# Kernel tuning notes

Hardware: AMD Instinct MI355X
Metric: run time of the kernel (lower is better)

## Reference

```python
import jax, jax.numpy as jnp
import numpy as np

B, H, N, D = 1, 24, 3072, 128
BM = 192            # query block size (kernel is hard-coded to BM=192)
QG = N // BM        # number of query groups
TOP_KEYS = 0.3
MULTIPLE_OF = 128
TK = int(MULTIPLE_OF * round(TOP_KEYS * N / MULTIPLE_OF))  # 896


def setup_inputs() -> dict:
    key = jax.random.key(0)
    kq, kk, kv = jax.random.split(key, 3)
    q = jax.random.normal(kq, (B, H, N, D), dtype=jnp.float32)
    k = jax.random.normal(kk, (B, H, N, D), dtype=jnp.float32)
    v = jax.random.normal(kv, (B, H, N, D), dtype=jnp.float32)
    return {"q": q, "k": k, "v": v}


def reference(q, k, v):
    """Full-step (inference_step==1) path of SparseDiffAttn._fast_attention:
    dense_colsum_attn -> top-k key selection per 192-query block -> csp_attn,
    returning o_cache = o_dense - o_sparse (the cached residual output)."""
    scale = 1.0 / jnp.sqrt(jnp.asarray(D, q.dtype))
    # --- dense_colsum_attn ---
    s = jnp.einsum('bhqd,bhkd->bhqk', q, k) * scale          # [B,H,N,N]
    p = jax.nn.softmax(s, axis=-1)                           # softmax probs
    o = jnp.einsum('bhqk,bhkd->bhqd', p, v)                  # dense output
    # block column sums: per 192-query group, sum of probs per key
    bs = p.reshape(B, H, QG, BM, N).sum(axis=3)              # [B,H,QG,N]
    # --- top-k routing (should_compress_indices=False branch) ---
    _, inds = jax.lax.top_k(jax.lax.stop_gradient(bs), TK)   # [B,H,QG,TK]
    # --- csp_attn: block-sparse attention over selected keys ---
    k_sel = jnp.take_along_axis(k[:, :, None], inds[..., None], axis=3)  # [B,H,QG,TK,D]
    v_sel = jnp.take_along_axis(v[:, :, None], inds[..., None], axis=3)
    qb = q.reshape(B, H, QG, BM, D)
    ss = jnp.einsum('bhgqd,bhgkd->bhgqk', qb, k_sel) * scale # [B,H,QG,BM,TK]
    ps = jax.nn.softmax(ss, axis=-1)
    o_sparse = jnp.einsum('bhgqk,bhgkd->bhgqd', ps, v_sel).reshape(B, H, N, D)
    # o_cache = o - csp_attn(q,k,v,inds,counts)
    return o - o_sparse
```

## Files before the change

kernel.cpp:

```cpp
#include <hip/hip_runtime.h>
#include <stdint.h>
#include <math.h>


#define H 24
#define N 3072
#define DH 128
#define SCALE 0.08838834764831845f
#define TK 896
#define MARG 1.6e-5f
#define MAXC 96

typedef __attribute__((ext_vector_type(8))) short short8;
typedef __attribute__((ext_vector_type(4))) float f32x4;
typedef __attribute__((address_space(1))) unsigned char GAS;
typedef __attribute__((address_space(3))) unsigned char LAS;
#define GLD16(g, l) __builtin_amdgcn_global_load_lds((GAS*)(g), (LAS*)(l), 16, 0, 0)

__device__ __forceinline__ uint32_t bf_rne(float x){
  uint32_t u = __float_as_uint(x);
  return (u + 0x7FFFu + ((u >> 16) & 1u)) >> 16;
}

__device__ __forceinline__ f32x4 f4zero(){ f32x4 z = {0.f,0.f,0.f,0.f}; return z; }

__device__ __forceinline__ void split8_2(const float* f, uint4& h4, uint4& l4){
  uint32_t hw[4], lw[4];
#pragma unroll
  for (int i = 0; i < 4; i++){
    float a = f[2*i], b = f[2*i+1];
    uint32_t ha = bf_rne(a), hb = bf_rne(b);
    float ra = a - __uint_as_float(ha << 16);
    float rb = b - __uint_as_float(hb << 16);
    hw[i] = ha | (hb << 16);
    lw[i] = bf_rne(ra) | (bf_rne(rb) << 16);
  }
  h4.x = hw[0]; h4.y = hw[1]; h4.z = hw[2]; h4.w = hw[3];
  l4.x = lw[0]; l4.y = lw[1]; l4.z = lw[2]; l4.w = lw[3];
}

__device__ __forceinline__ short8 as_s8(const uint4 u){
  union { uint4 u4; short8 s; } t; t.u4 = u; return t.s;
}

__device__ __forceinline__ void mapHC(int bid, int& h, int& ch){
  int x = bid & 7;
  int i = bid >> 3;
  h = x + 8 * (i / 48);
  ch = i % 48;
}

__device__ __forceinline__ void load_qfrags2(const float* qhead, int R, int w, int lane,
                                             uint4* qh, uint4* ql){
  int row = R + w*16 + (lane & 15);
  const float* qp = qhead + (size_t)row * DH;
#pragma unroll
  for (int s = 0; s < 4; s++){
    int d0 = s*32 + (lane >> 4)*8;
    float4 a = *(const float4*)(qp + d0);
    float4 b = *(const float4*)(qp + d0 + 4);
    float f[8] = {a.x*SCALE, a.y*SCALE, a.z*SCALE, a.w*SCALE,
                  b.x*SCALE, b.y*SCALE, b.z*SCALE, b.w*SCALE};
    split8_2(f, qh[s], ql[s]);
  }
}

__device__ __forceinline__ void ldK16(const float* kp, float4* r){
  r[0] = *(const float4*)(kp);
  r[1] = *(const float4*)(kp + 4);
  r[2] = *(const float4*)(kp + 8);
  r[3] = *(const float4*)(kp + 12);
}
__device__ __forceinline__ void wrK16(const float4* r, char* khi, char* klo,
                                      int jst, int dblk){
  float f0[8] = {r[0].x,r[0].y,r[0].z,r[0].w,r[1].x,r[1].y,r[1].z,r[1].w};
  float f1[8] = {r[2].x,r[2].y,r[2].z,r[2].w,r[3].x,r[3].y,r[3].z,r[3].w};
  uint4 h4, l4;
  int base = jst*256 + dblk*32;
  int sw = (jst & 7) << 4;
  split8_2(f0, h4, l4);
  *(uint4*)(khi + (base ^ sw)) = h4;
  *(uint4*)(klo + (base ^ sw)) = l4;
  split8_2(f1, h4, l4);
  *(uint4*)(khi + ((base + 16) ^ sw)) = h4;
  *(uint4*)(klo + ((base + 16) ^ sw)) = l4;
}

struct V16 { float4 a0, b0, a1, b1; };
__device__ __forceinline__ V16 load_v(const float* vp0, const float* vp1){
  V16 v;
  v.a0 = *(const float4*)(vp0);
  v.b0 = *(const float4*)(vp0 + 4);
  v.a1 = *(const float4*)(vp1);
  v.b1 = *(const float4*)(vp1 + 4);
  return v;
}
__device__ __forceinline__ void write_v(const V16& v, char* vts, int jv2, int dv8){
  float f0[8] = {v.a0.x,v.a0.y,v.a0.z,v.a0.w,v.b0.x,v.b0.y,v.b0.z,v.b0.w};
  float f1[8] = {v.a1.x,v.a1.y,v.a1.z,v.a1.w,v.b1.x,v.b1.y,v.b1.z,v.b1.w};
#pragma unroll
  for (int i = 0; i < 8; i++){
    uint32_t wrd = bf_rne(f0[i]) | (bf_rne(f1[i]) << 16);
    int r = dv8 + i;
    int off = (r*80 + jv2*2) ^ (((r >> 3) & 1) << 4);
    *(uint32_t*)(vts + off) = wrd;
  }
}

__device__ __forceinline__ void zcompute3(const char* khi, const char* klo,
                                          const uint4* qh, const uint4* ql,
                                          int lane, f32x4* zac){
  zac[0] = f4zero(); zac[1] = f4zero();
#pragma unroll
  for (int s = 0; s < 4; s++){
    short8 qa = as_s8(qh[s]);
    short8 qb = as_s8(ql[s]);
#pragma unroll
    for (int ct = 0; ct < 2; ct++){
      int key = ct*16 + (lane & 15);
      int off = (key*256 + (s*32 + (lane >> 4)*8)*2) ^ ((key & 7) << 4);
      short8 kh = *(const short8*)(khi + off);
      short8 kl = *(const short8*)(klo + off);
      zac[ct] = __builtin_amdgcn_mfma_f32_16x16x32_bf16(qa, kl, zac[ct], 0, 0, 0);
      zac[ct] = __builtin_amdgcn_mfma_f32_16x16x32_bf16(qb, kh, zac[ct], 0, 0, 0);
      zac[ct] = __builtin_amdgcn_mfma_f32_16x16x32_bf16(qa, kh, zac[ct], 0, 0, 0);
    }
  }
}

__device__ __forceinline__ void pv_step(const float pn[2][4], char* pw, const char* vts,
                                        f32x4* oac, int l15, int l4){
#pragma unroll
  for (int ct = 0; ct < 2; ct++)
#pragma unroll
    for (int r = 0; r < 4; r++){
      int row = l4*4 + r;
      int off = (row*80 + (ct*16 + l15)*2) ^ (((row >> 3) & 1) << 4);
      *(unsigned short*)(pw + off) = (unsigned short)bf_rne(pn[ct][r]);
    }
  int offA = (l15*80 + l4*16) ^ (((l15 >> 3) & 1) << 4);
  short8 ap = *(const short8*)(pw + offA);
#pragma unroll
  for (int vt = 0; vt < 8; vt++){
    int vrow = vt*16 + l15;
    int offB = (vrow*80 + l4*16) ^ (((vrow >> 3) & 1) << 4);
    short8 vb = *(const short8*)(vts + offB);
    oac[vt] = __builtin_amdgcn_mfma_f32_16x16x32_bf16(ap, vb, oac[vt], 0, 0, 0);
  }
}

__global__ __launch_bounds__(256) void kS(const float* __restrict__ kg,
                                          unsigned short* __restrict__ khig,
                                          unsigned short* __restrict__ klog){
  size_t idx = ((size_t)blockIdx.x*256 + threadIdx.x)*8;
  float4 a = *(const float4*)(kg + idx);
  float4 b = *(const float4*)(kg + idx + 4);
  float f[8] = {a.x,a.y,a.z,a.w,b.x,b.y,b.z,b.w};
  uint4 h4, l4;
  split8_2(f, h4, l4);
  *(uint4*)(khig + idx) = h4;
  *(uint4*)(klog + idx) = l4;
}

template<int DMA>
__global__ __launch_bounds__(256, 3) void kAB(const float* __restrict__ qg,
                                              const float* __restrict__ kg,
                                              const float* __restrict__ vg,
                                              const unsigned short* __restrict__ khig,
                                              const unsigned short* __restrict__ klog,
                                              double* __restrict__ Zg,
                                              float* __restrict__ cpart,
                                              float* __restrict__ outg){
  __shared__ alignas(16) char khi[2][8192];
  __shared__ alignas(16) char klo[2][8192];
  __shared__ alignas(16) char vts[10240];
  __shared__ alignas(16) char pls[4][1280];
  __shared__ float colbuf[2][4][32];
  int h, ch; mapHC(blockIdx.x, h, ch);
  const int tid = threadIdx.x, w = tid >> 6, lane = tid & 63;
  const int l15 = lane & 15, l4 = lane >> 4;
  const int R = ch * 64;
  const float* qhead = qg + (size_t)h*N*DH;
  const float* khead = kg + (size_t)h*N*DH;
  const float* vhead = vg + (size_t)h*N*DH;
  uint4 qh[4], ql[4];
  load_qfrags2(qhead, R, w, lane, qh, ql);

  size_t b0 = 0, b1 = 0;
  if (DMA){
    int g0 = w*128 + lane, g1 = g0 + 64;
    int k0 = g0 >> 4, sl0 = (g0 & 15) ^ (k0 & 7);
    int k1 = g1 >> 4, sl1 = (g1 & 15) ^ (k1 & 7);
    b0 = ((size_t)h*N + k0)*DH + sl0*8;
    b1 = ((size_t)h*N + k1)*DH + sl1*8;
  }
  const int wofs = w*2048;
  const int jst = tid >> 3, dblk = tid & 7;
  const int jv2 = (tid & 15)*2, dv8 = (tid >> 4)*8;

  if (DMA){
    GLD16(khig + b0, khi[0] + wofs);  GLD16(khig + b1, khi[0] + wofs + 1024);
    GLD16(klog + b0, klo[0] + wofs);  GLD16(klog + b1, klo[0] + wofs + 1024);
  } else {
    float4 k0r[4];
    ldK16(khead + (size_t)jst*DH + dblk*16, k0r);
    wrK16(k0r, khi[0], klo[0], jst, dblk);
  }
  __syncthreads();
  double zs[4] = {0.0,0.0,0.0,0.0};
  float4 kr[4];
  for (int kt = 0; kt < 96; kt++){
    int cur = kt & 1;
    if (kt < 95){
      if (DMA){
        size_t st = (size_t)(kt+1)*32*DH;
        GLD16(khig + b0 + st, khi[cur^1] + wofs);  GLD16(khig + b1 + st, khi[cur^1] + wofs + 1024);
        GLD16(klog + b0 + st, klo[cur^1] + wofs);  GLD16(klog + b1 + st, klo[cur^1] + wofs + 1024);
      } else {
        ldK16(khead + (size_t)((kt+1)*32 + jst)*DH + dblk*16, kr);
      }
    }
    f32x4 zac[2];
    zcompute3(khi[cur], klo[cur], qh, ql, lane, zac);
#pragma unroll
    for (int ct = 0; ct < 2; ct++)
#pragma unroll
      for (int r = 0; r < 4; r++)
        zs[r] += (double)__expf(zac[ct][r]);
    if (!DMA && kt < 95) wrK16(kr, khi[cur^1], klo[cur^1], jst, dblk);
    __syncthreads();
  }
#pragma unroll
  for (int m = 1; m < 16; m <<= 1)
#pragma unroll
    for (int r = 0; r < 4; r++)
      zs[r] += __shfl_xor(zs[r], m);
  float rz[4];
#pragma unroll
  for (int r = 0; r < 4; r++) rz[r] = (float)(1.0 / zs[r]);
  if (l15 == 0){
#pragma unroll
    for (int r = 0; r < 4; r++)
      Zg[h*N + R + w*16 + l4*4 + r] = zs[r];
  }

  if (DMA){
    GLD16(khig + b0, khi[0] + wofs);  GLD16(khig + b1, khi[0] + wofs + 1024);
    GLD16(klog + b0, klo[0] + wofs);  GLD16(klog + b1, klo[0] + wofs + 1024);
  } else {
    float4 k0r[4];
    ldK16(khead + (size_t)jst*DH + dblk*16, k0r);
    wrK16(k0r, khi[0], klo[0], jst, dblk);
  }
  {
    V16 v0 = load_v(vhead + (size_t)jv2*DH + dv8, vhead + (size_t)(jv2+1)*DH + dv8);
    write_v(v0, vts, jv2, dv8);
  }
  __syncthreads();
  f32x4 oac[8];
#pragma unroll
  for (int i = 0; i < 8; i++) oac[i] = f4zero();
  float* cp = cpart + (size_t)(h*48 + ch) * 3072;
  V16 vr;
  for (int kt = 0; kt < 96; kt++){
    int cur = kt & 1;
    if (kt > 0 && tid < 32)
      cp[(kt-1)*32 + tid] = colbuf[cur^1][0][tid] + colbuf[cur^1][1][tid]
                          + colbuf[cur^1][2][tid] + colbuf[cur^1][3][tid];
    if (kt < 95){
      if (DMA){
        size_t st = (size_t)(kt+1)*32*DH;
        GLD16(khig + b0 + st, khi[cur^1] + wofs);  GLD16(khig + b1 + st, khi[cur^1] + wofs + 1024);
        GLD16(klog + b0 + st, klo[cur^1] + wofs);  GLD16(klog + b1 + st, klo[cur^1] + wofs + 1024);
      } else {
        ldK16(khead + (size_t)((kt+1)*32 + jst)*DH + dblk*16, kr);
      }
      vr = load_v(vhead + (size_t)((kt+1)*32 + jv2)*DH + dv8,
                  vhead + (size_t)((kt+1)*32 + jv2 + 1)*DH + dv8);
    }
    f32x4 zac[2];
    zcompute3(khi[cur], klo[cur], qh, ql, lane, zac);
    float pn[2][4];
#pragma unroll
    for (int ct = 0; ct < 2; ct++)
#pragma unroll
      for (int r = 0; r < 4; r++)
        pn[ct][r] = __expf(zac[ct][r]) * rz[r];
#pragma unroll
    for (int ct = 0; ct < 2; ct++){
      float cs = pn[ct][0] + pn[ct][1] + pn[ct][2] + pn[ct][3];
      cs += __shfl_xor(cs, 16);
      cs += __shfl_xor(cs, 32);
      if (lane < 16) colbuf[cur][w][ct*16 + lane] = cs;
    }
    pv_step(pn, pls[w], vts, oac, l15, l4);
    __syncthreads();
    if (kt < 95){
      write_v(vr, vts, jv2, dv8);
      if (!DMA) wrK16(kr, khi[cur^1], klo[cur^1], jst, dblk);
    }
    __syncthreads();
  }
  if (tid < 32)
    cp[95*32 + tid] = colbuf[1][0][tid] + colbuf[1][1][tid]
                    + colbuf[1][2][tid] + colbuf[1][3][tid];
#pragma unroll
  for (int vt = 0; vt < 8; vt++)
#pragma unroll
    for (int r = 0; r < 4; r++)
      outg[((size_t)h*N + R + w*16 + l4*4 + r)*DH + vt*16 + l15] = oac[vt][r];
}

__global__ __launch_bounds__(256, 2) void kC(const float* __restrict__ cpart,
                                             const double* __restrict__ Zd,
                                             const float* __restrict__ qg,
                                             const float* __restrict__ kg,
                                             int* __restrict__ selg){
  __shared__ float cu[3072];
  __shared__ int red[4];
  __shared__ int runS;
  __shared__ int cidx[MAXC];
  __shared__ double cval[MAXC];
  __shared__ double rbuf[256];
  const int gid = blockIdx.x;
  const int h = gid >> 4, g = gid & 15;
  const int tid = threadIdx.x, w = tid >> 6, lane = tid & 63;
  const float* p0 = cpart + (size_t)(h*48 + g*3) * 3072;
  const float* p1 = p0 + 3072;
  const float* p2 = p0 + 6144;
  for (int i = tid; i < 3072; i += 256)
    cu[i] = p0[i] + p1[i] + p2[i];
  __syncthreads();
  uint32_t lo = 0u, hi = 0xFFFFFFFFu;
  for (int it = 0; it < 32; it++){
    bool active = (lo < hi);
    uint32_t mid = (uint32_t)(((uint64_t)lo + (uint64_t)hi + 1ull) >> 1);
    int c = 0;
    if (active){
      for (int i = tid; i < 3072; i += 256)
        c += (__float_as_uint(cu[i]) >= mid) ? 1 : 0;
#pragma unroll
      for (int m = 1; m < 64; m <<= 1) c += __shfl_xor(c, m);
    }
    if (lane == 0) red[w] = c;
    __syncthreads();
    int tot = red[0] + red[1] + red[2] + red[3];
    __syncthreads();
    if (active){ if (tot >= TK) lo = mid; else hi = mid - 1; }
  }
  const float Vf = __uint_as_float(lo);
  const float thr_hi = Vf + MARG;
  const float thr_lo = Vf - MARG;
  {
    int c = 0;
    for (int i = tid; i < 3072; i += 256) c += (cu[i] > thr_hi) ? 1 : 0;
#pragma unroll
    for (int m = 1; m < 64; m <<= 1) c += __shfl_xor(c, m);
    if (lane == 0) red[w] = c;
  }
  __syncthreads();
  const int n_in = red[0] + red[1] + red[2] + red[3];
  const int need = TK - n_in;
  int* sb = selg + (size_t)gid * TK;
  if (tid == 0) runS = 0;
  __syncthreads();
  for (int ck = 0; ck < 12; ck++){
    int j = ck*256 + tid;
    bool f = (cu[j] > thr_hi);
    unsigned long long bal = __ballot(f);
    int wpre = __popcll(bal & ((1ull << lane) - 1ull));
    int wtot = __popcll(bal);
    if (lane == 0) red[w] = wtot;
    __syncthreads();
    int woff = 0;
    for (int x = 0; x < w; x++) woff += red[x];
    int base = runS;
    if (f) sb[base + woff + wpre] = j;
    __syncthreads();
    if (tid == 0) runS = base + red[0] + red[1] + red[2] + red[3];
    __syncthreads();
  }
  if (tid == 0) runS = 0;
  __syncthreads();
  for (int ck = 0; ck < 12; ck++){
    int j = ck*256 + tid;
    bool f = (!(cu[j] > thr_hi)) && (cu[j] >= thr_lo);
    unsigned long long bal = __ballot(f);
    int wpre = __popcll(bal & ((1ull << lane) - 1ull));
    int wtot = __popcll(bal);
    if (lane == 0) red[w] = wtot;
    __syncthreads();
    int woff = 0;
    for (int x = 0; x < w; x++) woff += red[x];
    int base = runS;
    int pos = base + woff + wpre;
    if (f && pos < MAXC) cidx[pos] = j;
    __syncthreads();
    if (tid == 0) runS = base + red[0] + red[1] + red[2] + red[3];
    __syncthreads();
  }
  int ccnt = runS < MAXC ? runS : MAXC;
  __syncthreads();
  const int row = g*192 + (tid < 192 ? tid : 0);
  const float* qp = qg + ((size_t)h*N + row)*DH;
  const double Zrow = Zd[h*N + row];
  for (int c = 0; c < ccnt; c++){
    double t = 0.0;
    if (tid < 192){
      const float* kp = kg + ((size_t)h*N + cidx[c])*DH;
      double a0 = 0.0, a1 = 0.0, a2 = 0.0, a3 = 0.0;
#pragma unroll 4
      for (int d = 0; d < DH; d += 4){
        a0 = fma((double)qp[d],   (double)kp[d],   a0);
        a1 = fma((double)qp[d+1], (double)kp[d+1], a1);
        a2 = fma((double)qp[d+2], (double)kp[d+2], a2);
        a3 = fma((double)qp[d+3], (double)kp[d+3], a3);
      }
      double z = ((a0 + a1) + (a2 + a3)) * 0.08838834764831845;
      t = exp(z) / Zrow;
    }
    rbuf[tid] = t;
    __syncthreads();
#pragma unroll
    for (int s = 128; s > 0; s >>= 1){
      if (tid < s) rbuf[tid] += rbuf[tid + s];
      __syncthreads();
    }
    if (tid == 0) cval[c] = rbuf[0];
    __syncthreads();
  }
  if (tid < ccnt){
    double my = cval[tid];
    int myi = cidx[tid];
    int rank = 0;
    for (int u = 0; u < ccnt; u++){
      double cu_ = cval[u];
      if (cu_ > my || (cu_ == my && cidx[u] < myi)) rank++;
    }
    if (rank < need) sb[n_in + rank] = myi;
  }
}

template<int DMA>
__global__ __launch_bounds__(256, 3) void kD(const float* __restrict__ qg,
                                             const float* __restrict__ kg,
                                             const float* __restrict__ vg,
                                             const double* __restrict__ Zg,
                                             const int* __restrict__ selg,
                                             const unsigned short* __restrict__ khig,
                                             const unsigned short* __restrict__ klog,
                                             float* __restrict__ outg){
  __shared__ alignas(16) char khi[2][8192];
  __shared__ alignas(16) char klo[2][8192];
  __shared__ alignas(16) char vts[10240];
  __shared__ alignas(16) char pls[4][1280];
  __shared__ int sell[TK];
  int h, ch; mapHC(blockIdx.x, h, ch);
  const int tid = threadIdx.x, w = tid >> 6, lane = tid & 63;
  const int l15 = lane & 15, l4 = lane >> 4;
  const int R = ch * 64;
  const int g = ch / 3;
  const float* qhead = qg + (size_t)h*N*DH;
  const float* khead = kg + (size_t)h*N*DH;
  const float* vhead = vg + (size_t)h*N*DH;
  const int* sb = selg + (size_t)(h*16 + g) * TK;
  for (int i = tid; i < TK; i += 256) sell[i] = sb[i];
  uint4 qh[4], ql[4];
  load_qfrags2(qhead, R, w, lane, qh, ql);
  float rz[4];
#pragma unroll
  for (int r = 0; r < 4; r++)
    rz[r] = (float)(1.0 / Zg[h*N + R + w*16 + l4*4 + r]);
  f32x4 oac[8];
#pragma unroll
  for (int i = 0; i < 8; i++) oac[i] = f4zero();
  float rh[4] = {0.f,0.f,0.f,0.f};

  int p0g = 0, p1g = 0, sl0 = 0, sl1 = 0;
  if (DMA){
    int g0 = w*128 + lane, g1 = g0 + 64;
    p0g = g0 >> 4; sl0 = (g0 & 15) ^ (p0g & 7);
    p1g = g1 >> 4; sl1 = (g1 & 15) ^ (p1g & 7);
  }
  const int wofs = w*2048;
  const int jst = tid >> 3, dblk = tid & 7;
  const int jv2 = (tid & 15)*2, dv8 = (tid >> 4)*8;
  __syncthreads();
  if (DMA){
    size_t b0 = ((size_t)h*N + sell[p0g])*DH + sl0*8;
    size_t b1 = ((size_t)h*N + sell[p1g])*DH + sl1*8;
    GLD16(khig + b0, khi[0] + wofs);  GLD16(khig + b1, khi[0] + wofs + 1024);
    GLD16(klog + b0, klo[0] + wofs);  GLD16(klog + b1, klo[0] + wofs + 1024);
  } else {
    float4 k0r[4];
    ldK16(khead + (size_t)sell[jst]*DH + dblk*16, k0r);
    wrK16(k0r, khi[0], klo[0], jst, dblk);
  }
  {
    V16 v0 = load_v(vhead + (size_t)sell[jv2]*DH + dv8,
                    vhead + (size_t)sell[jv2+1]*DH + dv8);
    write_v(v0, vts, jv2, dv8);
  }
  __syncthreads();
  float4 kr[4];
  V16 vr;
  for (int st = 0; st < 28; st++){
    int cur = st & 1;
    if (st < 27){
      if (DMA){
        size_t b0 = ((size_t)h*N + sell[(st+1)*32 + p0g])*DH + sl0*8;
        size_t b1 = ((size_t)h*N + sell[(st+1)*32 + p1g])*DH + sl1*8;
        GLD16(khig + b0, khi[cur^1] + wofs);  GLD16(khig + b1, khi[cur^1] + wofs + 1024);
        GLD16(klog + b0, klo[cur^1] + wofs);  GLD16(klog + b1, klo[cur^1] + wofs + 1024);
      } else {
        ldK16(khead + (size_t)sell[(st+1)*32 + jst]*DH + dblk*16, kr);
      }
      vr = load_v(vhead + (size_t)sell[(st+1)*32 + jv2]*DH + dv8,
                  vhead + (size_t)sell[(st+1)*32 + jv2 + 1]*DH + dv8);
    }
    f32x4 zac[2];
    zcompute3(khi[cur], klo[cur], qh, ql, lane, zac);
    float pn[2][4];
#pragma unroll
    for (int ct = 0; ct < 2; ct++)
#pragma unroll
      for (int r = 0; r < 4; r++){
        pn[ct][r] = __expf(zac[ct][r]) * rz[r];
        rh[r] += pn[ct][r];
      }
    pv_step(pn, pls[w], vts, oac, l15, l4);
    __syncthreads();
    if (st < 27){
      write_v(vr, vts, jv2, dv8);
      if (!DMA) wrK16(kr, khi[cur^1], klo[cur^1], jst, dblk);
    }
    __syncthreads();
  }
#pragma unroll
  for (int m = 1; m < 16; m <<= 1)
#pragma unroll
    for (int r = 0; r < 4; r++)
      rh[r] += __shfl_xor(rh[r], m);
  float ri[4];
#pragma unroll
  for (int r = 0; r < 4; r++) ri[r] = 1.0f / rh[r];
#pragma unroll
  for (int vt = 0; vt < 8; vt++)
#pragma unroll
    for (int r = 0; r < 4; r++){
      size_t idx = ((size_t)h*N + R + w*16 + l4*4 + r)*DH + vt*16 + l15;
      outg[idx] = outg[idx] - oac[vt][r]*ri[r];
    }
}

extern "C" void kernel_launch(void* const* d_in, const int* in_sizes, int n_in,
                              void* d_out, int out_size, void* d_ws, size_t ws_size,
                              hipStream_t stream){
  (void)in_sizes; (void)n_in; (void)out_size;
  const float* q = (const float*)d_in[0];
  const float* k = (const float*)d_in[1];
  const float* v = (const float*)d_in[2];
  float* out = (float*)d_out;
  const size_t KELEMS = (size_t)H*N*DH;
  const size_t KBYTES = KELEMS*2;
  const size_t ZB = (size_t)H*N*8;
  const size_t CPB = (size_t)1152*3072*4;
  const size_t SELB = (size_t)384*TK*4;
  const bool dma = ws_size >= 2*KBYTES + ZB + CPB + SELB;
  char* wsb = (char*)d_ws;
  unsigned short *khig = nullptr, *klog = nullptr;
  double* Z; float* cpart; int* sel;
  if (dma){
    khig = (unsigned short*)wsb;
    klog = (unsigned short*)(wsb + KBYTES);
    Z = (double*)(wsb + 2*KBYTES);
    cpart = (float*)(wsb + 2*KBYTES + ZB);
    sel = (int*)(wsb + 2*KBYTES + ZB + CPB);
  } else {
    Z = (double*)wsb;
    cpart = (float*)(wsb + ZB);
    sel = (int*)(wsb + ZB + CPB);
  }
  if (dma){
    kS<<<dim3(4608), dim3(256), 0, stream>>>(k, khig, klog);
    kAB<1><<<dim3(1152), dim3(256), 0, stream>>>(q, k, v, khig, klog, Z, cpart, out);
    kC<<<dim3(384), dim3(256), 0, stream>>>(cpart, Z, q, k, sel);
    kD<1><<<dim3(1152), dim3(256), 0, stream>>>(q, k, v, Z, sel, khig, klog, out);
  } else {
    kAB<0><<<dim3(1152), dim3(256), 0, stream>>>(q, k, v, khig, klog, Z, cpart, out);
    kC<<<dim3(384), dim3(256), 0, stream>>>(cpart, Z, q, k, sel);
    kD<0><<<dim3(1152), dim3(256), 0, stream>>>(q, k, v, Z, sel, khig, klog, out);
  }
}
```

Before: 851.6 us.

## Process two query tiles per block, precast V to bf16, drop K-lo in PV passes

kAB now handles 128 query rows per block (two 64-row tiles sharing each K/V tile load), halving the grid and reusing LDS traffic. V is pre-converted to bf16 in the split kernel. The probability-times-V passes in kAB and kD use only two MFMAs per score instead of three because the K low part is dropped. The selection margin is widened to absorb the extra error. Occupancy bounds change too (kAB to 2, kD to 4), trading register pressure and precision for fewer MFMAs and fewer loads.

```diff
diff --git a/kernel.cpp b/kernel.cpp
--- a/kernel.cpp
+++ b/kernel.cpp
@@ -8,7 +8,7 @@
 #define DH 128
 #define SCALE 0.08838834764831845f
 #define TK 896
-#define MARG 1.6e-5f
+#define MARG 1.0e-4f
 #define MAXC 96
 
 typedef __attribute__((ext_vector_type(8))) short short8;
@@ -43,7 +43,13 @@
   union { uint4 u4; short8 s; } t; t.u4 = u; return t.s;
 }
 
-__device__ __forceinline__ void mapHC(int bid, int& h, int& ch){
+__device__ __forceinline__ void mapHC24(int bid, int& h, int& ch){
+  int x = bid & 7;
+  int i = bid >> 3;
+  h = x + 8 * (i / 24);
+  ch = i % 24;
+}
+__device__ __forceinline__ void mapHC48(int bid, int& h, int& ch){
   int x = bid & 7;
   int i = bid >> 3;
   h = x + 8 * (i / 48);
@@ -85,6 +91,20 @@
   *(uint4*)(khi + ((base + 16) ^ sw)) = h4;
   *(uint4*)(klo + ((base + 16) ^ sw)) = l4;
 }
+__device__ __forceinline__ void wrK16h(const float4* r, char* khi, int jst, int dblk){
+  float f[16] = {r[0].x,r[0].y,r[0].z,r[0].w,r[1].x,r[1].y,r[1].z,r[1].w,
+                 r[2].x,r[2].y,r[2].z,r[2].w,r[3].x,r[3].y,r[3].z,r[3].w};
+  uint32_t wv[8];
+#pragma unroll
+  for (int i = 0; i < 8; i++)
+    wv[i] = bf_rne(f[2*i]) | (bf_rne(f[2*i+1]) << 16);
+  int base = jst*256 + dblk*32;
+  int sw = (jst & 7) << 4;
+  uint4 a = {wv[0],wv[1],wv[2],wv[3]};
+  uint4 b = {wv[4],wv[5],wv[6],wv[7]};
+  *(uint4*)(khi + (base ^ sw)) = a;
+  *(uint4*)(khi + ((base + 16) ^ sw)) = b;
+}
 
 struct V16 { float4 a0, b0, a1, b1; };
 __device__ __forceinline__ V16 load_v(const float* vp0, const float* vp1){
@@ -106,25 +126,103 @@
     *(uint32_t*)(vts + off) = wrd;
   }
 }
-
-__device__ __forceinline__ void zcompute3(const char* khi, const char* klo,
-                                          const uint4* qh, const uint4* ql,
-                                          int lane, f32x4* zac){
-  zac[0] = f4zero(); zac[1] = f4zero();
+__device__ __forceinline__ void write_vbf(uint4 va, uint4 vb, char* vts, int jv2, int dv8){
+  const unsigned short* a = (const unsigned short*)&va;
+  const unsigned short* b = (const unsigned short*)&vb;
+#pragma unroll
+  for (int i = 0; i < 8; i++){
+    uint32_t wrd = (uint32_t)a[i] | ((uint32_t)b[i] << 16);
+    int r = dv8 + i;
+    int off = (r*80 + jv2*2) ^ (((r >> 3) & 1) << 4);
+    *(uint32_t*)(vts + off) = wrd;
+  }
+}
+
+__device__ __forceinline__ void zc3_dual(const char* khi, const char* klo,
+    const uint4* qhA, const uint4* qlA, const uint4* qhB, const uint4* qlB,
+    int lane, f32x4* zA, f32x4* zB){
+  zA[0] = f4zero(); zA[1] = f4zero();
+  zB[0] = f4zero(); zB[1] = f4zero();
 #pragma unroll
   for (int s = 0; s < 4; s++){
-    short8 qa = as_s8(qh[s]);
-    short8 qb = as_s8(ql[s]);
+    short8 qaA = as_s8(qhA[s]), qbA = as_s8(qlA[s]);
+    short8 qaB = as_s8(qhB[s]), qbB = as_s8(qlB[s]);
 #pragma unroll
     for (int ct = 0; ct < 2; ct++){
       int key = ct*16 + (lane & 15);
       int off = (key*256 + (s*32 + (lane >> 4)*8)*2) ^ ((key & 7) << 4);
       short8 kh = *(const short8*)(khi + off);
       short8 kl = *(const short8*)(klo + off);
-      zac[ct] = __builtin_amdgcn_mfma_f32_16x16x32_bf16(qa, kl, zac[ct], 0, 0, 0);
+      zA[ct] = __builtin_amdgcn_mfma_f32_16x16x32_bf16(qaA, kl, zA[ct], 0, 0, 0);
+      zA[ct] = __builtin_amdgcn_mfma_f32_16x16x32_bf16(qbA, kh, zA[ct], 0, 0, 0);
+      zA[ct] = __builtin_amdgcn_mfma_f32_16x16x32_bf16(qaA, kh, zA[ct], 0, 0, 0);
+      zB[ct] = __builtin_amdgcn_mfma_f32_16x16x32_bf16(qaB, kl, zB[ct], 0, 0, 0);
+      zB[ct] = __builtin_amdgcn_mfma_f32_16x16x32_bf16(qbB, kh, zB[ct], 0, 0, 0);
+      zB[ct] = __builtin_amdgcn_mfma_f32_16x16x32_bf16(qaB, kh, zB[ct], 0, 0, 0);
+    }
+  }
+}
+
+__device__ __forceinline__ void zc2_dual(const char* khi,
+    const uint4* qhA, const uint4* qlA, const uint4* qhB, const uint4* qlB,
+    int lane, f32x4* zA, f32x4* zB){
+  zA[0] = f4zero(); zA[1] = f4zero();
+  zB[0] = f4zero(); zB[1] = f4zero();
+#pragma unroll
+  for (int s = 0; s < 4; s++){
+    short8 qaA = as_s8(qhA[s]), qbA = as_s8(qlA[s]);
+    short8 qaB = as_s8(qhB[s]), qbB = as_s8(qlB[s]);
+#pragma unroll
+    for (int ct = 0; ct < 2; ct++){
+      int key = ct*16 + (lane & 15);
+      int off = (key*256 + (s*32 + (lane >> 4)*8)*2) ^ ((key & 7) << 4);
+      short8 kh = *(const short8*)(khi + off);
+      zA[ct] = __builtin_amdgcn_mfma_f32_16x16x32_bf16(qbA, kh, zA[ct], 0, 0, 0);
+      zA[ct] = __builtin_amdgcn_mfma_f32_16x16x32_bf16(qaA, kh, zA[ct], 0, 0, 0);
+      zB[ct] = __builtin_amdgcn_mfma_f32_16x16x32_bf16(qbB, kh, zB[ct], 0, 0, 0);
+      zB[ct] = __builtin_amdgcn_mfma_f32_16x16x32_bf16(qaB, kh, zB[ct], 0, 0, 0);
+    }
+  }
+}
+
+__device__ __forceinline__ void zc2_one(const char* khi,
+    const uint4* qh, const uint4* ql, int lane, f32x4* zac){
+  zac[0] = f4zero(); zac[1] = f4zero();
+#pragma unroll
+  for (int s = 0; s < 4; s++){
+    short8 qa = as_s8(qh[s]), qb = as_s8(ql[s]);
+#pragma unroll
+    for (int ct = 0; ct < 2; ct++){
+      int key = ct*16 + (lane & 15);
+      int off = (key*256 + (s*32 + (lane >> 4)*8)*2) ^ ((key & 7) << 4);
+      short8 kh = *(const short8*)(khi + off);
       zac[ct] = __builtin_amdgcn_mfma_f32_16x16x32_bf16(qb, kh, zac[ct], 0, 0, 0);
       zac[ct] = __builtin_amdgcn_mfma_f32_16x16x32_bf16(qa, kh, zac[ct], 0, 0, 0);
     }
+  }
+}
+
+__device__ __forceinline__ void pv_dual(const float pnA[2][4], const float pnB[2][4],
+    char* pwA, char* pwB, const char* vts, f32x4* oacA, f32x4* oacB, int l15, int l4){
+#pragma unroll
+  for (int ct = 0; ct < 2; ct++)
+#pragma unroll
+    for (int r = 0; r < 4; r++){
+      int row = l4*4 + r;
+      int off = (row*80 + (ct*16 + l15)*2) ^ (((row >> 3) & 1) << 4);
+      *(unsigned short*)(pwA + off) = (unsigned short)bf_rne(pnA[ct][r]);
+      *(unsigned short*)(pwB + off) = (unsigned short)bf_rne(pnB[ct][r]);
+    }
+  int offA = (l15*80 + l4*16) ^ (((l15 >> 3) & 1) << 4);
+  short8 apA = *(const short8*)(pwA + offA);
+  short8 apB = *(const short8*)(pwB + offA);
+#pragma unroll
+  for (int vt = 0; vt < 8; vt++){
+    int vrow = vt*16 + l15;
+    int offB = (vrow*80 + l4*16) ^ (((vrow >> 3) & 1) << 4);
+    short8 vb = *(const short8*)(vts + offB);
+    oacA[vt] = __builtin_amdgcn_mfma_f32_16x16x32_bf16(apA, vb, oacA[vt], 0, 0, 0);
+    oacB[vt] = __builtin_amdgcn_mfma_f32_16x16x32_bf16(apB, vb, oacB[vt], 0, 0, 0);
   }
 }
 
@@ -150,8 +248,10 @@
 }
 
 __global__ __launch_bounds__(256) void kS(const float* __restrict__ kg,
+                                          const float* __restrict__ vg,
                                           unsigned short* __restrict__ khig,
-                                          unsigned short* __restrict__ klog){
+                                          unsigned short* __restrict__ klog,
+                                          unsigned short* __restrict__ vbfg){
   size_t idx = ((size_t)blockIdx.x*256 + threadIdx.x)*8;
   float4 a = *(const float4*)(kg + idx);
   float4 b = *(const float4*)(kg + idx + 4);
@@ -160,31 +260,40 @@
   split8_2(f, h4, l4);
   *(uint4*)(khig + idx) = h4;
   *(uint4*)(klog + idx) = l4;
+  float4 c = *(const float4*)(vg + idx);
+  float4 d = *(const float4*)(vg + idx + 4);
+  uint4 v4;
+  v4.x = bf_rne(c.x) | (bf_rne(c.y) << 16);
+  v4.y = bf_rne(c.z) | (bf_rne(c.w) << 16);
+  v4.z = bf_rne(d.x) | (bf_rne(d.y) << 16);
+  v4.w = bf_rne(d.z) | (bf_rne(d.w) << 16);
+  *(uint4*)(vbfg + idx) = v4;
 }
 
 template<int DMA>
-__global__ __launch_bounds__(256, 3) void kAB(const float* __restrict__ qg,
+__global__ __launch_bounds__(256, 2) void kAB(const float* __restrict__ qg,
                                               const float* __restrict__ kg,
                                               const float* __restrict__ vg,
                                               const unsigned short* __restrict__ khig,
                                               const unsigned short* __restrict__ klog,
+                                              const unsigned short* __restrict__ vbfg,
                                               double* __restrict__ Zg,
                                               float* __restrict__ cpart,
                                               float* __restrict__ outg){
   __shared__ alignas(16) char khi[2][8192];
-  __shared__ alignas(16) char klo[2][8192];
+  __shared__ alignas(16) char kloB[16384];
   __shared__ alignas(16) char vts[10240];
-  __shared__ alignas(16) char pls[4][1280];
   __shared__ float colbuf[2][4][32];
-  int h, ch; mapHC(blockIdx.x, h, ch);
+  int h, ch; mapHC24(blockIdx.x, h, ch);
   const int tid = threadIdx.x, w = tid >> 6, lane = tid & 63;
   const int l15 = lane & 15, l4 = lane >> 4;
-  const int R = ch * 64;
+  const int R = ch * 128;
   const float* qhead = qg + (size_t)h*N*DH;
   const float* khead = kg + (size_t)h*N*DH;
   const float* vhead = vg + (size_t)h*N*DH;
-  uint4 qh[4], ql[4];
-  load_qfrags2(qhead, R, w, lane, qh, ql);
+  uint4 qhA[4], qlA[4], qhB[4], qlB[4];
+  load_qfrags2(qhead, R,      w, lane, qhA, qlA);
+  load_qfrags2(qhead, R + 64, w, lane, qhB, qlB);
 
   size_t b0 = 0, b1 = 0;
   if (DMA){
@@ -197,118 +306,142 @@
   const int wofs = w*2048;
   const int jst = tid >> 3, dblk = tid & 7;
   const int jv2 = (tid & 15)*2, dv8 = (tid >> 4)*8;
+  char* kloT0 = kloB;
+  char* kloT1 = kloB + 8192;
 
   if (DMA){
     GLD16(khig + b0, khi[0] + wofs);  GLD16(khig + b1, khi[0] + wofs + 1024);
-    GLD16(klog + b0, klo[0] + wofs);  GLD16(klog + b1, klo[0] + wofs + 1024);
+    GLD16(klog + b0, kloT0 + wofs);   GLD16(klog + b1, kloT0 + wofs + 1024);
   } else {
     float4 k0r[4];
     ldK16(khead + (size_t)jst*DH + dblk*16, k0r);
-    wrK16(k0r, khi[0], klo[0], jst, dblk);
-  }
-  __syncthreads();
-  double zs[4] = {0.0,0.0,0.0,0.0};
+    wrK16(k0r, khi[0], kloT0, jst, dblk);
+  }
+  __syncthreads();
+  double zsA[4] = {0.0,0.0,0.0,0.0};
+  double zsB[4] = {0.0,0.0,0.0,0.0};
   float4 kr[4];
+  for (int kt = 0; kt < 96; kt++){
+    int cur = kt & 1;
+    char* kloC = cur ? kloT1 : kloT0;
+    char* kloN = cur ? kloT0 : kloT1;
+    if (kt < 95){
+      if (DMA){
+        size_t st = (size_t)(kt+1)*32*DH;
+        GLD16(khig + b0 + st, khi[cur^1] + wofs);  GLD16(khig + b1 + st, khi[cur^1] + wofs + 1024);
+        GLD16(klog + b0 + st, kloN + wofs);        GLD16(klog + b1 + st, kloN + wofs + 1024);
+      } else {
+        ldK16(khead + (size_t)((kt+1)*32 + jst)*DH + dblk*16, kr);
+      }
+    }
+    f32x4 zA[2], zB[2];
+    zc3_dual(khi[cur], kloC, qhA, qlA, qhB, qlB, lane, zA, zB);
+#pragma unroll
+    for (int ct = 0; ct < 2; ct++)
+#pragma unroll
+      for (int r = 0; r < 4; r++){
+        zsA[r] += (double)__expf(zA[ct][r]);
+        zsB[r] += (double)__expf(zB[ct][r]);
+      }
+    if (!DMA && kt < 95) wrK16(kr, khi[cur^1], kloN, jst, dblk);
+    __syncthreads();
+  }
+#pragma unroll
+  for (int m = 1; m < 16; m <<= 1)
+#pragma unroll
+    for (int r = 0; r < 4; r++){
+      zsA[r] += __shfl_xor(zsA[r], m);
+      zsB[r] += __shfl_xor(zsB[r], m);
+    }
+  float rzA[4], rzB[4];
+#pragma unroll
+  for (int r = 0; r < 4; r++){
+    rzA[r] = (float)(1.0 / zsA[r]);
+    rzB[r] = (float)(1.0 / zsB[r]);
+  }
+  if (l15 == 0){
+#pragma unroll
+    for (int r = 0; r < 4; r++){
+      Zg[h*N + R      + w*16 + l4*4 + r] = zsA[r];
+      Zg[h*N + R + 64 + w*16 + l4*4 + r] = zsB[r];
+    }
+  }
+
+  char* pwA = kloB + w*2560;
+  char* pwB = pwA + 1280;
+  if (DMA){
+    GLD16(khig + b0, khi[0] + wofs);  GLD16(khig + b1, khi[0] + wofs + 1024);
+    uint4 va0 = *(const uint4*)(vbfg + ((size_t)h*N + jv2    )*DH + dv8);
+    uint4 vb0 = *(const uint4*)(vbfg + ((size_t)h*N + jv2 + 1)*DH + dv8);
+    write_vbf(va0, vb0, vts, jv2, dv8);
+  } else {
+    float4 k0r[4];
+    ldK16(khead + (size_t)jst*DH + dblk*16, k0r);
+    wrK16h(k0r, khi[0], jst, dblk);
+    V16 v0 = load_v(vhead + (size_t)jv2*DH + dv8, vhead + (size_t)(jv2+1)*DH + dv8);
+    write_v(v0, vts, jv2, dv8);
+  }
+  __syncthreads();
+  f32x4 oacA[8], oacB[8];
+#pragma unroll
+  for (int i = 0; i < 8; i++){ oacA[i] = f4zero(); oacB[i] = f4zero(); }
+  uint4 va, vb2;
+  V16 vr;
   for (int kt = 0; kt < 96; kt++){
     int cur = kt & 1;
     if (kt < 95){
       if (DMA){
         size_t st = (size_t)(kt+1)*32*DH;
         GLD16(khig + b0 + st, khi[cur^1] + wofs);  GLD16(khig + b1 + st, khi[cur^1] + wofs + 1024);
-        GLD16(klog + b0 + st, klo[cur^1] + wofs);  GLD16(klog + b1 + st, klo[cur^1] + wofs + 1024);
+        va  = *(const uint4*)(vbfg + ((size_t)h*N + (kt+1)*32 + jv2    )*DH + dv8);
+        vb2 = *(const uint4*)(vbfg + ((size_t)h*N + (kt+1)*32 + jv2 + 1)*DH + dv8);
       } else {
         ldK16(khead + (size_t)((kt+1)*32 + jst)*DH + dblk*16, kr);
+        vr = load_v(vhead + (size_t)((kt+1)*32 + jv2)*DH + dv8,
+                    vhead + (size_t)((kt+1)*32 + jv2 + 1)*DH + dv8);
       }
     }
-    f32x4 zac[2];
-    zcompute3(khi[cur], klo[cur], qh, ql, lane, zac);
+    f32x4 zA[2], zB[2];
+    zc2_dual(khi[cur], qhA, qlA, qhB, qlB, lane, zA, zB);
+    float pnA[2][4], pnB[2][4];
 #pragma unroll
     for (int ct = 0; ct < 2; ct++)
 #pragma unroll
-      for (int r = 0; r < 4; r++)
-        zs[r] += (double)__expf(zac[ct][r]);
-    if (!DMA && kt < 95) wrK16(kr, khi[cur^1], klo[cur^1], jst, dblk);
-    __syncthreads();
-  }
-#pragma unroll
-  for (int m = 1; m < 16; m <<= 1)
-#pragma unroll
-    for (int r = 0; r < 4; r++)
-      zs[r] += __shfl_xor(zs[r], m);
-  float rz[4];
-#pragma unroll
-  for (int r = 0; r < 4; r++) rz[r] = (float)(1.0 / zs[r]);
-  if (l15 == 0){
-#pragma unroll
-    for (int r = 0; r < 4; r++)
-      Zg[h*N + R + w*16 + l4*4 + r] = zs[r];
-  }
-
-  if (DMA){
-    GLD16(khig + b0, khi[0] + wofs);  GLD16(khig + b1, khi[0] + wofs + 1024);
-    GLD16(klog + b0, klo[0] + wofs);  GLD16(klog + b1, klo[0] + wofs + 1024);
-  } else {
-    float4 k0r[4];
-    ldK16(khead + (size_t)jst*DH + dblk*16, k0r);
-    wrK16(k0r, khi[0], klo[0], jst, dblk);
-  }
-  {
-    V16 v0 = load_v(vhead + (size_t)jv2*DH + dv8, vhead + (size_t)(jv2+1)*DH + dv8);
-    write_v(v0, vts, jv2, dv8);
-  }
-  __syncthreads();
-  f32x4 oac[8];
-#pragma unroll
-  for (int i = 0; i < 8; i++) oac[i] = f4zero();
-  float* cp = cpart + (size_t)(h*48 + ch) * 3072;
-  V16 vr;
-  for (int kt = 0; kt < 96; kt++){
-    int cur = kt & 1;
-    if (kt > 0 && tid < 32)
-      cp[(kt-1)*32 + tid] = colbuf[cur^1][0][tid] + colbuf[cur^1][1][tid]
-                          + colbuf[cur^1][2][tid] + colbuf[cur^1][3][tid];
+      for (int r = 0; r < 4; r++){
+        pnA[ct][r] = __expf(zA[ct][r]) * rzA[r];
+        pnB[ct][r] = __expf(zB[ct][r]) * rzB[r];
+      }
+#pragma unroll
+    for (int ct = 0; ct < 2; ct++){
+      float csA = pnA[ct][0] + pnA[ct][1] + pnA[ct][2] + pnA[ct][3];
+      float csB = pnB[ct][0] + pnB[ct][1] + pnB[ct][2] + pnB[ct][3];
+      csA += __shfl_xor(csA, 16);  csA += __shfl_xor(csA, 32);
+      csB += __shfl_xor(csB, 16);  csB += __shfl_xor(csB, 32);
+      if (lane < 16){
+        colbuf[0][w][ct*16 + lane] = csA;
+        colbuf[1][w][ct*16 + lane] = csB;
+      }
+    }
+    pv_dual(pnA, pnB, pwA, pwB, vts, oacA, oacB, l15, l4);
+    __syncthreads();
+    if (tid < 64){
+      int a = tid >> 5, c = tid & 31;
+      cpart[(size_t)(h*48 + ch*2 + a)*3072 + kt*32 + c] =
+        colbuf[a][0][c] + colbuf[a][1][c] + colbuf[a][2][c] + colbuf[a][3][c];
+    }
     if (kt < 95){
-      if (DMA){
-        size_t st = (size_t)(kt+1)*32*DH;
-        GLD16(khig + b0 + st, khi[cur^1] + wofs);  GLD16(khig + b1 + st, khi[cur^1] + wofs + 1024);
-        GLD16(klog + b0 + st, klo[cur^1] + wofs);  GLD16(klog + b1 + st, klo[cur^1] + wofs + 1024);
-      } else {
-        ldK16(khead + (size_t)((kt+1)*32 + jst)*DH + dblk*16, kr);
-      }
-      vr = load_v(vhead + (size_t)((kt+1)*32 + jv2)*DH + dv8,
-                  vhead + (size_t)((kt+1)*32 + jv2 + 1)*DH + dv8);
-    }
-    f32x4 zac[2];
-    zcompute3(khi[cur], klo[cur], qh, ql, lane, zac);
-    float pn[2][4];
-#pragma unroll
-    for (int ct = 0; ct < 2; ct++)
-#pragma unroll
-      for (int r = 0; r < 4; r++)
-        pn[ct][r] = __expf(zac[ct][r]) * rz[r];
-#pragma unroll
-    for (int ct = 0; ct < 2; ct++){
-      float cs = pn[ct][0] + pn[ct][1] + pn[ct][2] + pn[ct][3];
-      cs += __shfl_xor(cs, 16);
-      cs += __shfl_xor(cs, 32);
-      if (lane < 16) colbuf[cur][w][ct*16 + lane] = cs;
-    }
-    pv_step(pn, pls[w], vts, oac, l15, l4);
-    __syncthreads();
-    if (kt < 95){
-      write_v(vr, vts, jv2, dv8);
-      if (!DMA) wrK16(kr, khi[cur^1], klo[cur^1], jst, dblk);
-    }
-    __syncthreads();
-  }
-  if (tid < 32)
-    cp[95*32 + tid] = colbuf[1][0][tid] + colbuf[1][1][tid]
-                    + colbuf[1][2][tid] + colbuf[1][3][tid];
+      if (DMA) write_vbf(va, vb2, vts, jv2, dv8);
+      else { write_v(vr, vts, jv2, dv8); wrK16h(kr, khi[cur^1], jst, dblk); }
+    }
+    __syncthreads();
+  }
 #pragma unroll
   for (int vt = 0; vt < 8; vt++)
 #pragma unroll
-    for (int r = 0; r < 4; r++)
-      outg[((size_t)h*N + R + w*16 + l4*4 + r)*DH + vt*16 + l15] = oac[vt][r];
+    for (int r = 0; r < 4; r++){
+      outg[((size_t)h*N + R      + w*16 + l4*4 + r)*DH + vt*16 + l15] = oacA[vt][r];
+      outg[((size_t)h*N + R + 64 + w*16 + l4*4 + r)*DH + vt*16 + l15] = oacB[vt][r];
+    }
 }
 
 __global__ __launch_bounds__(256, 2) void kC(const float* __restrict__ cpart,
@@ -442,20 +575,19 @@
 }
 
 template<int DMA>
-__global__ __launch_bounds__(256, 3) void kD(const float* __restrict__ qg,
+__global__ __launch_bounds__(256, 4) void kD(const float* __restrict__ qg,
                                              const float* __restrict__ kg,
                                              const float* __restrict__ vg,
                                              const double* __restrict__ Zg,
                                              const int* __restrict__ selg,
                                              const unsigned short* __restrict__ khig,
-                                             const unsigned short* __restrict__ klog,
+                                             const unsigned short* __restrict__ vbfg,
                                              float* __restrict__ outg){
   __shared__ alignas(16) char khi[2][8192];
-  __shared__ alignas(16) char klo[2][8192];
   __shared__ alignas(16) char vts[10240];
   __shared__ alignas(16) char pls[4][1280];
   __shared__ int sell[TK];
-  int h, ch; mapHC(blockIdx.x, h, ch);
+  int h, ch; mapHC48(blockIdx.x, h, ch);
   const int tid = threadIdx.x, w = tid >> 6, lane = tid & 63;
   const int l15 = lane & 15, l4 = lane >> 4;
   const int R = ch * 64;
@@ -490,13 +622,13 @@
     size_t b0 = ((size_t)h*N + sell[p0g])*DH + sl0*8;
     size_t b1 = ((size_t)h*N + sell[p1g])*DH + sl1*8;
     GLD16(khig + b0, khi[0] + wofs);  GLD16(khig + b1, khi[0] + wofs + 1024);
-    GLD16(klog + b0, klo[0] + wofs);  GLD16(klog + b1, klo[0] + wofs + 1024);
+    uint4 va0 = *(const uint4*)(vbfg + ((size_t)h*N + sell[jv2]    )*DH + dv8);
+    uint4 vb0 = *(const uint4*)(vbfg + ((size_t)h*N + sell[jv2 + 1])*DH + dv8);
+    write_vbf(va0, vb0, vts, jv2, dv8);
   } else {
     float4 k0r[4];
     ldK16(khead + (size_t)sell[jst]*DH + dblk*16, k0r);
-    wrK16(k0r, khi[0], klo[0], jst, dblk);
-  }
-  {
+    wrK16h(k0r, khi[0], jst, dblk);
     V16 v0 = load_v(vhead + (size_t)sell[jv2]*DH + dv8,
                     vhead + (size_t)sell[jv2+1]*DH + dv8);
     write_v(v0, vts, jv2, dv8);
@@ -504,6 +636,7 @@
   __syncthreads();
   float4 kr[4];
   V16 vr;
+  uint4 va, vb2;
   for (int st = 0; st < 28; st++){
     int cur = st & 1;
     if (st < 27){
@@ -511,15 +644,16 @@
         size_t b0 = ((size_t)h*N + sell[(st+1)*32 + p0g])*DH + sl0*8;
         size_t b1 = ((size_t)h*N + sell[(st+1)*32 + p1g])*DH + sl1*8;
         GLD16(khig + b0, khi[cur^1] + wofs);  GLD16(khig + b1, khi[cur^1] + wofs + 1024);
-        GLD16(klog + b0, klo[cur^1] + wofs);  GLD16(klog + b1, klo[cur^1] + wofs + 1024);
+        va  = *(const uint4*)(vbfg + ((size_t)h*N + sell[(st+1)*32 + jv2    ])*DH + dv8);
+        vb2 = *(const uint4*)(vbfg + ((size_t)h*N + sell[(st+1)*32 + jv2 + 1])*DH + dv8);
       } else {
         ldK16(khead + (size_t)sell[(st+1)*32 + jst]*DH + dblk*16, kr);
+        vr = load_v(vhead + (size_t)sell[(st+1)*32 + jv2]*DH + dv8,
+                    vhead + (size_t)sell[(st+1)*32 + jv2 + 1]*DH + dv8);
       }
-      vr = load_v(vhead + (size_t)sell[(st+1)*32 + jv2]*DH + dv8,
-                  vhead + (size_t)sell[(st+1)*32 + jv2 + 1]*DH + dv8);
     }
     f32x4 zac[2];
-    zcompute3(khi[cur], klo[cur], qh, ql, lane, zac);
+    zc2_one(khi[cur], qh, ql, lane, zac);
     float pn[2][4];
 #pragma unroll
     for (int ct = 0; ct < 2; ct++)
@@ -531,8 +665,8 @@
     pv_step(pn, pls[w], vts, oac, l15, l4);
     __syncthreads();
     if (st < 27){
-      write_v(vr, vts, jv2, dv8);
-      if (!DMA) wrK16(kr, khi[cur^1], klo[cur^1], jst, dblk);
+      if (DMA) write_vbf(va, vb2, vts, jv2, dv8);
+      else { write_v(vr, vts, jv2, dv8); wrK16h(kr, khi[cur^1], jst, dblk); }
     }
     __syncthreads();
   }
@@ -566,29 +700,30 @@
   const size_t ZB = (size_t)H*N*8;
   const size_t CPB = (size_t)1152*3072*4;
   const size_t SELB = (size_t)384*TK*4;
-  const bool dma = ws_size >= 2*KBYTES + ZB + CPB + SELB;
+  const bool dma = ws_size >= 3*KBYTES + ZB + CPB + SELB;
   char* wsb = (char*)d_ws;
-  unsigned short *khig = nullptr, *klog = nullptr;
+  unsigned short *khig = nullptr, *klog = nullptr, *vbfg = nullptr;
   double* Z; float* cpart; int* sel;
   if (dma){
     khig = (unsigned short*)wsb;
     klog = (unsigned short*)(wsb + KBYTES);
-    Z = (double*)(wsb + 2*KBYTES);
-    cpart = (float*)(wsb + 2*KBYTES + ZB);
-    sel = (int*)(wsb + 2*KBYTES + ZB + CPB);
+    vbfg = (unsigned short*)(wsb + 2*KBYTES);
+    Z = (double*)(wsb + 3*KBYTES);
+    cpart = (float*)(wsb + 3*KBYTES + ZB);
+    sel = (int*)(wsb + 3*KBYTES + ZB + CPB);
   } else {
     Z = (double*)wsb;
     cpart = (float*)(wsb + ZB);
     sel = (int*)(wsb + ZB + CPB);
   }
   if (dma){
-    kS<<<dim3(4608), dim3(256), 0, stream>>>(k, khig, klog);
-    kAB<1><<<dim3(1152), dim3(256), 0, stream>>>(q, k, v, khig, klog, Z, cpart, out);
+    kS<<<dim3(4608), dim3(256), 0, stream>>>(k, v, khig, klog, vbfg);
+    kAB<1><<<dim3(576), dim3(256), 0, stream>>>(q, k, v, khig, klog, vbfg, Z, cpart, out);
     kC<<<dim3(384), dim3(256), 0, stream>>>(cpart, Z, q, k, sel);
-    kD<1><<<dim3(1152), dim3(256), 0, stream>>>(q, k, v, Z, sel, khig, klog, out);
+    kD<1><<<dim3(1152), dim3(256), 0, stream>>>(q, k, v, Z, sel, khig, vbfg, out);
   } else {
-    kAB<0><<<dim3(1152), dim3(256), 0, stream>>>(q, k, v, khig, klog, Z, cpart, out);
+    kAB<0><<<dim3(576), dim3(256), 0, stream>>>(q, k, v, khig, klog, vbfg, Z, cpart, out);
     kC<<<dim3(384), dim3(256), 0, stream>>>(cpart, Z, q, k, sel);
-    kD<0><<<dim3(1152), dim3(256), 0, stream>>>(q, k, v, Z, sel, khig, klog, out);
-  }
-}
+    kD<0><<<dim3(1152), dim3(256), 0, stream>>>(q, k, v, Z, sel, khig, vbfg, out);
+  }
+}
```

After: 1.004 ms. +17.9%, slower.
